# Performance work log

Hardware: AMD Instinct MI355X
Metric: run time of the kernel (lower is better)

## Reference

```python
import jax, jax.numpy as jnp
import numpy as np

B, N, HID = 4, 2048, 1024
QKV, NH = 1024, 16
HD = QKV // NH


def setup_inputs() -> dict:
    key = jax.random.key(0)
    ks = jax.random.split(key, 5)
    s = 1.0 / np.sqrt(HID)
    x = jax.random.normal(ks[0], (B, N, HID), dtype=jnp.float32)
    Wq = jax.random.normal(ks[1], (HID, QKV), dtype=jnp.float32) * s
    Wk = jax.random.normal(ks[2], (HID, QKV), dtype=jnp.float32) * s
    Wv = jax.random.normal(ks[3], (HID, QKV), dtype=jnp.float32) * s
    Wo = jax.random.normal(ks[4], (QKV, HID), dtype=jnp.float32) * (1.0 / np.sqrt(QKV))
    return {"x": x, "Wq": Wq, "Wk": Wk, "Wv": Wv, "Wo": Wo}


def reference(x, Wq, Wk, Wv, Wo):
    # Projections: [B, N, QKV]
    q = x @ Wq
    k = x @ Wk
    v = x @ Wv
    # Split heads -> [B, NH, N, HD]
    def split(t):
        return t.reshape(B, N, NH, HD).transpose(0, 2, 1, 3)
    q, k, v = split(q), split(k), split(v)
    # NOTE: original scales by 1/sqrt(qkv_dim) (full dim), not head_dim
    q = q * (1.0 / jnp.sqrt(jnp.float32(QKV)))
    scores = jnp.einsum("bhqd,bhkd->bhqk", q, k)  # [B, NH, N, N]
    attn = jax.nn.softmax(scores, axis=-1)
    out = jnp.einsum("bhqk,bhkd->bhqd", attn, v)  # [B, NH, N, HD]
    out = out.transpose(0, 2, 1, 3).reshape(B, N, QKV)
    return out @ Wo
```

## Files before the change

### kernel.cpp

```cpp
#include <hip/hip_runtime.h>

typedef unsigned short u16;
typedef unsigned int u32;
typedef __attribute__((ext_vector_type(8))) short bf16x8;
typedef __attribute__((ext_vector_type(4))) float f32x4;
typedef __attribute__((ext_vector_type(16))) float f32x16;

#define L2E 1.44269504088896340736f

__device__ __forceinline__ u16 f2bf(float f) {
  unsigned u = __float_as_uint(f);
  u += 0x7FFF + ((u >> 16) & 1u);
  return (u16)(u >> 16);
}

__device__ __forceinline__ u32 cvtpk(float lo, float hi) {
  u32 r;
  asm("v_cvt_pk_bf16_f32 %0, %1, %2" : "=v"(r) : "v"(lo), "v"(hi));
  return r;
}

__device__ __forceinline__ void gload_lds16(const u16* g, u16* lds) {
  __builtin_amdgcn_global_load_lds(
      (const __attribute__((address_space(1))) void*)g,
      (__attribute__((address_space(3))) void*)lds, 16, 0, 0);
}

__global__ __launch_bounds__(256) void k_cvt(const float* __restrict__ in,
                                             u16* __restrict__ out) {
  const int i = (blockIdx.x * 256 + threadIdx.x) * 4;
  float4 a = *(const float4*)(in + i);
  ushort4 o;
  o.x = f2bf(a.x); o.y = f2bf(a.y); o.z = f2bf(a.z); o.w = f2bf(a.w);
  *(ushort4*)(out + i) = o;
}

__global__ __launch_bounds__(256) void k_tw(
    const float* __restrict__ w0, const float* __restrict__ w1,
    const float* __restrict__ w2, const float* __restrict__ w3,
    u16* __restrict__ o0, u16* __restrict__ o1,
    u16* __restrict__ o2, u16* __restrict__ o3) {
  __shared__ float t[64][65];
  const float* W = blockIdx.z == 0 ? w0 : blockIdx.z == 1 ? w1 : blockIdx.z == 2 ? w2 : w3;
  u16* O = blockIdx.z == 0 ? o0 : blockIdx.z == 1 ? o1 : blockIdx.z == 2 ? o2 : o3;
  const int nb = blockIdx.x * 64, kb = blockIdx.y * 64;
  const int lx = threadIdx.x & 63, ly = threadIdx.x >> 6;
  for (int r = ly; r < 64; r += 4)
    t[r][lx] = W[(size_t)(kb + r) * 1024 + nb + lx];
  __syncthreads();
  for (int r = ly; r < 64; r += 4)
    O[(size_t)(nb + r) * 1024 + kb + lx] = f2bf(t[lx][r]);
}

__device__ __forceinline__ void gemm_core(const u16* __restrict__ Ag,
                                          const u16* __restrict__ Bg,
                                          f32x4 acc[4][4]) {
  __shared__ u16 As[4096], Bs[4096];
  const int tid = threadIdx.x;
  const int lane = tid & 63, wv = tid >> 6;
  const size_t row0 = (size_t)blockIdx.y * 128;
  const size_t col0 = (size_t)blockIdx.x * 128;
  const int rA0 = wv * 32 + (lane >> 2);
  const int rA1 = rA0 + 16;
  const int kk = (lane & 3) * 8;
  const int wr = (wv >> 1) * 64, wc = (wv & 1) * 64;
  const int fr = lane & 15, fk = (lane >> 4) * 8;
#pragma unroll
  for (int m = 0; m < 4; m++)
#pragma unroll
    for (int n = 0; n < 4; n++)
      acc[m][n] = {0.f, 0.f, 0.f, 0.f};

  for (int kt = 0; kt < 32; kt++) {
    const int k0 = kt * 32;
    gload_lds16(Ag + (row0 + rA0) * 1024 + k0 + kk, &As[(wv * 2 + 0) * 512]);
    gload_lds16(Ag + (row0 + rA1) * 1024 + k0 + kk, &As[(wv * 2 + 1) * 512]);
    gload_lds16(Bg + (col0 + rA0) * 1024 + k0 + kk, &Bs[(wv * 2 + 0) * 512]);
    gload_lds16(Bg + (col0 + rA1) * 1024 + k0 + kk, &Bs[(wv * 2 + 1) * 512]);
    __syncthreads();
    bf16x8 af[4], bfr[4];
#pragma unroll
    for (int m = 0; m < 4; m++)
      af[m] = *(const bf16x8*)&As[(wr + m * 16 + fr) * 32 + fk];
#pragma unroll
    for (int n = 0; n < 4; n++)
      bfr[n] = *(const bf16x8*)&Bs[(wc + n * 16 + fr) * 32 + fk];
#pragma unroll
    for (int m = 0; m < 4; m++)
#pragma unroll
      for (int n = 0; n < 4; n++)
        acc[m][n] = __builtin_amdgcn_mfma_f32_16x16x32_bf16(af[m], bfr[n], acc[m][n], 0, 0, 0);
    __syncthreads();
  }
}

__global__ __launch_bounds__(256) void k_proj(
    const u16* __restrict__ xb, const u16* __restrict__ wqT,
    const u16* __restrict__ wkT, const u16* __restrict__ wvT,
    u16* __restrict__ q, u16* __restrict__ k, u16* __restrict__ v) {
  f32x4 acc[4][4];
  const int z = blockIdx.z;
  const u16* Bg = z == 0 ? wqT : z == 1 ? wkT : wvT;
  gemm_core(xb, Bg, acc);
  const int lane = threadIdx.x & 63, wv = threadIdx.x >> 6;
  const int wr = (wv >> 1) * 64, wc = (wv & 1) * 64;
  const int rb = blockIdx.y * 128 + wr + ((lane >> 4) * 4);
  const int cb = blockIdx.x * 128 + wc + (lane & 15);
#pragma unroll
  for (int m = 0; m < 4; m++) {
#pragma unroll
    for (int n = 0; n < 4; n++) {
      const int C = cb + n * 16;
      const int h = C >> 6, d = C & 63;
      if (z == 2) {
        const int R = rb + m * 16;
        const int b = R >> 11, nn = R & 2047;
        ushort4 o;
        o.x = f2bf(acc[m][n][0]); o.y = f2bf(acc[m][n][1]);
        o.z = f2bf(acc[m][n][2]); o.w = f2bf(acc[m][n][3]);
        *(ushort4*)&v[(size_t)((b * 16 + h) * 64 + d) * 2048 + nn] = o;
      } else {
        u16* dst = (z == 0) ? q : k;
        const float s = (z == 0) ? (0.03125f * L2E) : 1.0f;
#pragma unroll
        for (int i = 0; i < 4; i++) {
          const int R = rb + m * 16 + i;
          const int b = R >> 11, nn = R & 2047;
          dst[(size_t)((b * 16 + h) * 2048 + nn) * 64 + d] = f2bf(acc[m][n][i] * s);
        }
      }
    }
  }
}

__global__ __launch_bounds__(256) void k_out(const u16* __restrict__ att,
                                             const u16* __restrict__ woT,
                                             float* __restrict__ out) {
  f32x4 acc[4][4];
  gemm_core(att, woT, acc);
  const int lane = threadIdx.x & 63, wv = threadIdx.x >> 6;
  const int wr = (wv >> 1) * 64, wc = (wv & 1) * 64;
  const int rb = blockIdx.y * 128 + wr + ((lane >> 4) * 4);
  const int cb = blockIdx.x * 128 + wc + (lane & 15);
#pragma unroll
  for (int m = 0; m < 4; m++)
#pragma unroll
    for (int n = 0; n < 4; n++)
#pragma unroll
      for (int i = 0; i < 4; i++)
        out[(size_t)(rb + m * 16 + i) * 1024 + cb + n * 16] = acc[m][n][i];
}

__global__ __launch_bounds__(256, 2) void k_attn(const u16* __restrict__ q,
                                                 const u16* __restrict__ k,
                                                 const u16* __restrict__ v,
                                                 u16* __restrict__ att) {
  __shared__ u16 SM[16384];
  const int lane = threadIdx.x & 63, wv = threadIdx.x >> 6;
  const int lo5 = lane & 31, hi = lane >> 5;
  const int r7 = lo5 & 7;
  const int bh = blockIdx.y;
  const int b = bh >> 4, h = bh & 15;
  const int q0w = blockIdx.x * 128 + wv * 32;
  const size_t base = (size_t)bh * 2048 * 64;

  const int l0 = wv * 64 + lane, l1 = 256 + l0;
  const int sr0 = l0 >> 3, sc0 = ((l0 & 7) ^ (sr0 & 7)) * 8;
  const int sr1 = l1 >> 3, sc1 = ((l1 & 7) ^ (sr1 & 7)) * 8;

  bf16x8 qb[4];
  {
    const u16* qp = q + base + (size_t)(q0w + lo5) * 64 + hi * 8;
#pragma unroll
    for (int db = 0; db < 4; db++) qb[db] = *(const bf16x8*)(qp + db * 16);
  }

  f32x16 o0, o1;
#pragma unroll
  for (int i = 0; i < 16; i++) { o0[i] = 0.f; o1[i] = 0.f; }
  float m_run = -3.0e38f, l_run = 0.f;

  {
    u16* Kd = SM;
    u16* Vd = SM + 4096;
    gload_lds16(k + base + (size_t)sr0 * 64 + sc0, Kd + wv * 512);
    gload_lds16(k + base + (size_t)sr1 * 64 + sc1, Kd + 2048 + wv * 512);
    gload_lds16(v + base + (size_t)sr0 * 2048 + sc0, Vd + wv * 512);
    gload_lds16(v + base + (size_t)sr1 * 2048 + sc1, Vd + 2048 + wv * 512);
  }
  __syncthreads();

  int cur = 0;
  for (int kt = 0; kt < 32; kt++) {
    const int kb = kt * 64;
    {
      const int nkb = (kt + 1 < 32 ? kt + 1 : 0) * 64;
      u16* Kd = SM + (cur ^ 1) * 8192;
      u16* Vd = Kd + 4096;
      gload_lds16(k + base + (size_t)(nkb + sr0) * 64 + sc0, Kd + wv * 512);
      gload_lds16(k + base + (size_t)(nkb + sr1) * 64 + sc1, Kd + 2048 + wv * 512);
      gload_lds16(v + base + (size_t)sr0 * 2048 + nkb + sc0, Vd + wv * 512);
      gload_lds16(v + base + (size_t)sr1 * 2048 + nkb + sc1, Vd + 2048 + wv * 512);
    }

    const u16* Kc = SM + cur * 8192;
    const u16* Vc = Kc + 4096;

    f32x16 s0, s1;
#pragma unroll
    for (int i = 0; i < 16; i++) { s0[i] = 0.f; s1[i] = 0.f; }
    __builtin_amdgcn_s_setprio(1);
#pragma unroll
    for (int db = 0; db < 4; db++) {
      const int swz = ((db * 2 + hi) ^ r7) << 3;
      const bf16x8 k0 = *(const bf16x8*)&Kc[lo5 * 64 + swz];
      const bf16x8 k1 = *(const bf16x8*)&Kc[(32 + lo5) * 64 + swz];
      s0 = __builtin_amdgcn_mfma_f32_32x32x16_bf16(k0, qb[db], s0, 0, 0, 0);
      s1 = __builtin_amdgcn_mfma_f32_32x32x16_bf16(k1, qb[db], s1, 0, 0, 0);
    }
    __builtin_amdgcn_s_setprio(0);

    float t[16];
#pragma unroll
    for (int i = 0; i < 16; i++) t[i] = fmaxf(s0[i], s1[i]);
#pragma unroll
    for (int off = 8; off; off >>= 1)
#pragma unroll
      for (int i = 0; i < off; i++) t[i] = fmaxf(t[i], t[i + off]);
    const float tmax = fmaxf(t[0], __shfl_xor(t[0], 32, 64));

    const bool skip = __all(tmax - m_run <= 8.0f);
    float sc = 1.0f;
    if (!skip) {
      const float mnew = fmaxf(m_run, tmax);
      sc = exp2f(m_run - mnew);
      m_run = mnew;
    }

    float p0[16], p1[16];
#pragma unroll
    for (int i = 0; i < 16; i++) {
      p0[i] = exp2f(s0[i] - m_run);
      p1[i] = exp2f(s1[i] - m_run);
    }
    float u[16];
#pragma unroll
    for (int i = 0; i < 16; i++) u[i] = p0[i] + p1[i];
#pragma unroll
    for (int off = 8; off; off >>= 1)
#pragma unroll
      for (int i = 0; i < off; i++) u[i] += u[i + off];
    const float rs = u[0] + __shfl_xor(u[0], 32, 64);
    l_run = l_run * sc + rs;
    if (!skip) {
#pragma unroll
      for (int i = 0; i < 16; i++) { o0[i] *= sc; o1[i] *= sc; }
    }

    bf16x8 pa[4];
#pragma unroll
    for (int kh = 0; kh < 2; kh++) {
      const float* pp = kh ? p1 : p0;
#pragma unroll
      for (int kl = 0; kl < 2; kl++) {
        const int r0 = kl * 8;
        const u32 a0 = cvtpk(pp[r0 + 0], pp[r0 + 1]);
        const u32 a1 = cvtpk(pp[r0 + 2], pp[r0 + 3]);
        const u32 b0 = cvtpk(pp[r0 + 4], pp[r0 + 5]);
        const u32 b1 = cvtpk(pp[r0 + 6], pp[r0 + 7]);
        const u32 a0x = (u32)__shfl_xor((int)a0, 32, 64);
        const u32 a1x = (u32)__shfl_xor((int)a1, 32, 64);
        const u32 b0x = (u32)__shfl_xor((int)b0, 32, 64);
        const u32 b1x = (u32)__shfl_xor((int)b1, 32, 64);
        union { u32 w[4]; bf16x8 v; } U;
        U.w[0] = hi ? b0x : a0;
        U.w[1] = hi ? b1x : a1;
        U.w[2] = hi ? b0 : a0x;
        U.w[3] = hi ? b1 : a1x;
        pa[kh * 2 + kl] = U.v;
      }
    }

    __builtin_amdgcn_s_setprio(1);
#pragma unroll
    for (int ks = 0; ks < 4; ks++) {
      const int swz = ((ks * 2 + hi) ^ r7) << 3;
      const bf16x8 v0 = *(const bf16x8*)&Vc[lo5 * 64 + swz];
      const bf16x8 v1 = *(const bf16x8*)&Vc[(32 + lo5) * 64 + swz];
      o0 = __builtin_amdgcn_mfma_f32_32x32x16_bf16(v0, pa[ks], o0, 0, 0, 0);
      o1 = __builtin_amdgcn_mfma_f32_32x32x16_bf16(v1, pa[ks], o1, 0, 0, 0);
    }
    __builtin_amdgcn_s_setprio(0);

    __syncthreads();
    cur ^= 1;
  }

  const float linv = 1.0f / l_run;
  u16* W = SM + wv * 2176;
#pragma unroll
  for (int r = 0; r < 16; r++) {
    const int dd = (r & 3) + 8 * (r >> 2) + 4 * hi;
    W[lo5 * 68 + dd] = f2bf(o0[r] * linv);
    W[lo5 * 68 + 32 + dd] = f2bf(o1[r] * linv);
  }
  const int q_loc = lane >> 1, dh = (lane & 1) * 32;
  u16* dst = att + (size_t)(b * 2048 + q0w + q_loc) * 1024 + h * 64 + dh;
#pragma unroll
  for (int c = 0; c < 4; c++) {
    bf16x8 val = *(const bf16x8*)&W[q_loc * 68 + dh + c * 8];
    *(bf16x8*)(dst + c * 8) = val;
  }
}

extern "C" void kernel_launch(void* const* d_in, const int* in_sizes, int n_in,
                              void* d_out, int out_size, void* d_ws, size_t ws_size,
                              hipStream_t stream) {
  const float* x  = (const float*)d_in[0];
  const float* Wq = (const float*)d_in[1];
  const float* Wk = (const float*)d_in[2];
  const float* Wv = (const float*)d_in[3];
  const float* Wo = (const float*)d_in[4];
  float* out = (float*)d_out;

  char* ws = (char*)d_ws;
  u16* xb  = (u16*)ws; ws += (size_t)8192 * 1024 * 2;
  u16* wqT = (u16*)ws; ws += (size_t)1024 * 1024 * 2;
  u16* wkT = (u16*)ws; ws += (size_t)1024 * 1024 * 2;
  u16* wvT = (u16*)ws; ws += (size_t)1024 * 1024 * 2;
  u16* woT = (u16*)ws; ws += (size_t)1024 * 1024 * 2;
  u16* qb  = (u16*)ws; ws += (size_t)8192 * 1024 * 2;
  u16* kb  = (u16*)ws; ws += (size_t)8192 * 1024 * 2;
  u16* vb  = (u16*)ws; ws += (size_t)8192 * 1024 * 2;
  u16* att = (u16*)ws; ws += (size_t)8192 * 1024 * 2;

  k_cvt<<<dim3(8192), dim3(256), 0, stream>>>(x, xb);
  k_tw<<<dim3(16, 16, 4), dim3(256), 0, stream>>>(Wq, Wk, Wv, Wo, wqT, wkT, wvT, woT);
  k_proj<<<dim3(8, 64, 3), dim3(256), 0, stream>>>(xb, wqT, wkT, wvT, qb, kb, vb);
  k_attn<<<dim3(16, 64), dim3(256), 0, stream>>>(qb, kb, vb, att);
  k_out<<<dim3(8, 64), dim3(256), 0, stream>>>(att, woT, out);
}
```

Baseline: 351.9 us.

## Pre-tile K/V in LDS-ready layout, defer row-sum reduction, use native exp2

The QKV projection now writes K and V into a pre-tiled, fragment-ordered layout for each 64-key block. The attention kernel can then fetch each tile with contiguous global-to-LDS loads and read MFMA operands with simple strided offsets, with no XOR swizzle. The softmax denominator is kept as 16 per-lane partial sums and reduced only once after the loop, which removes a reduction tree and shuffle from every iteration. exp2f is replaced with the hardware exp2 builtin. The main risk is LDS bank conflicts from the unswizzled strided reads.

```diff
diff --git a/kernel.cpp b/kernel.cpp
--- a/kernel.cpp
+++ b/kernel.cpp
@@ -115,18 +115,30 @@
       if (z == 2) {
         const int R = rb + m * 16;
         const int b = R >> 11, nn = R & 2047;
+        const int bh = b * 16 + h;
         ushort4 o;
         o.x = f2bf(acc[m][n][0]); o.y = f2bf(acc[m][n][1]);
         o.z = f2bf(acc[m][n][2]); o.w = f2bf(acc[m][n][3]);
-        *(ushort4*)&v[(size_t)((b * 16 + h) * 64 + d) * 2048 + nn] = o;
-      } else {
-        u16* dst = (z == 0) ? q : k;
-        const float s = (z == 0) ? (0.03125f * L2E) : 1.0f;
+        const size_t off = (size_t)bh * 131072 + (size_t)(nn >> 6) * 4096 +
+                           ((nn & 63) >> 3) * 512 + d * 8 + (nn & 7);
+        *(ushort4*)&v[off] = o;
+      } else if (z == 1) {
 #pragma unroll
         for (int i = 0; i < 4; i++) {
           const int R = rb + m * 16 + i;
           const int b = R >> 11, nn = R & 2047;
-          dst[(size_t)((b * 16 + h) * 2048 + nn) * 64 + d] = f2bf(acc[m][n][i] * s);
+          const int bh = b * 16 + h;
+          const size_t off = (size_t)bh * 131072 + (size_t)(nn >> 6) * 4096 +
+                             (d >> 3) * 512 + (nn & 63) * 8 + (d & 7);
+          k[off] = f2bf(acc[m][n][i]);
+        }
+      } else {
+        const float s = 0.03125f * L2E;
+#pragma unroll
+        for (int i = 0; i < 4; i++) {
+          const int R = rb + m * 16 + i;
+          const int b = R >> 11, nn = R & 2047;
+          q[(size_t)((b * 16 + h) * 2048 + nn) * 64 + d] = f2bf(acc[m][n][i] * s);
         }
       }
     }
@@ -151,26 +163,24 @@
         out[(size_t)(rb + m * 16 + i) * 1024 + cb + n * 16] = acc[m][n][i];
 }
 
-__global__ __launch_bounds__(256, 2) void k_attn(const u16* __restrict__ q,
-                                                 const u16* __restrict__ k,
-                                                 const u16* __restrict__ v,
+__global__ __launch_bounds__(256, 2) void k_attn(const u16* __restrict__ qg,
+                                                 const u16* __restrict__ kg,
+                                                 const u16* __restrict__ vg,
                                                  u16* __restrict__ att) {
   __shared__ u16 SM[16384];
-  const int lane = threadIdx.x & 63, wv = threadIdx.x >> 6;
+  const int tid = threadIdx.x;
+  const int lane = tid & 63, wv = tid >> 6;
   const int lo5 = lane & 31, hi = lane >> 5;
-  const int r7 = lo5 & 7;
   const int bh = blockIdx.y;
   const int b = bh >> 4, h = bh & 15;
   const int q0w = blockIdx.x * 128 + wv * 32;
-  const size_t base = (size_t)bh * 2048 * 64;
-
-  const int l0 = wv * 64 + lane, l1 = 256 + l0;
-  const int sr0 = l0 >> 3, sc0 = ((l0 & 7) ^ (sr0 & 7)) * 8;
-  const int sr1 = l1 >> 3, sc1 = ((l1 & 7) ^ (sr1 & 7)) * 8;
+  const size_t qbase = (size_t)bh * 2048 * 64;
+  const u16* kt0 = kg + (size_t)bh * 131072;
+  const u16* vt0 = vg + (size_t)bh * 131072;
 
   bf16x8 qb[4];
   {
-    const u16* qp = q + base + (size_t)(q0w + lo5) * 64 + hi * 8;
+    const u16* qp = qg + qbase + (size_t)(q0w + lo5) * 64 + hi * 8;
 #pragma unroll
     for (int db = 0; db < 4; db++) qb[db] = *(const bf16x8*)(qp + db * 16);
   }
@@ -178,32 +188,31 @@
   f32x16 o0, o1;
 #pragma unroll
   for (int i = 0; i < 16; i++) { o0[i] = 0.f; o1[i] = 0.f; }
-  float m_run = -3.0e38f, l_run = 0.f;
-
-  {
-    u16* Kd = SM;
-    u16* Vd = SM + 4096;
-    gload_lds16(k + base + (size_t)sr0 * 64 + sc0, Kd + wv * 512);
-    gload_lds16(k + base + (size_t)sr1 * 64 + sc1, Kd + 2048 + wv * 512);
-    gload_lds16(v + base + (size_t)sr0 * 2048 + sc0, Vd + wv * 512);
-    gload_lds16(v + base + (size_t)sr1 * 2048 + sc1, Vd + 2048 + wv * 512);
-  }
+  float m_run = -3.0e38f;
+  float l16[16];
+#pragma unroll
+  for (int i = 0; i < 16; i++) l16[i] = 0.f;
+
+  gload_lds16(kt0 + (size_t)tid * 8, SM + wv * 512);
+  gload_lds16(kt0 + (size_t)(256 + tid) * 8, SM + 2048 + wv * 512);
+  gload_lds16(vt0 + (size_t)tid * 8, SM + 4096 + wv * 512);
+  gload_lds16(vt0 + (size_t)(256 + tid) * 8, SM + 6144 + wv * 512);
   __syncthreads();
 
   int cur = 0;
-  for (int kt = 0; kt < 32; kt++) {
-    const int kb = kt * 64;
+  for (int t = 0; t < 32; t++) {
     {
-      const int nkb = (kt + 1 < 32 ? kt + 1 : 0) * 64;
+      const int nt = (t + 1) & 31;
+      const u16* ks = kt0 + (size_t)nt * 4096;
+      const u16* vs = vt0 + (size_t)nt * 4096;
       u16* Kd = SM + (cur ^ 1) * 8192;
-      u16* Vd = Kd + 4096;
-      gload_lds16(k + base + (size_t)(nkb + sr0) * 64 + sc0, Kd + wv * 512);
-      gload_lds16(k + base + (size_t)(nkb + sr1) * 64 + sc1, Kd + 2048 + wv * 512);
-      gload_lds16(v + base + (size_t)sr0 * 2048 + nkb + sc0, Vd + wv * 512);
-      gload_lds16(v + base + (size_t)sr1 * 2048 + nkb + sc1, Vd + 2048 + wv * 512);
-    }
-
-    const u16* Kc = SM + cur * 8192;
+      gload_lds16(ks + (size_t)tid * 8, Kd + wv * 512);
+      gload_lds16(ks + (size_t)(256 + tid) * 8, Kd + 2048 + wv * 512);
+      gload_lds16(vs + (size_t)tid * 8, Kd + 4096 + wv * 512);
+      gload_lds16(vs + (size_t)(256 + tid) * 8, Kd + 6144 + wv * 512);
+    }
+
+    const u16* Kc = SM + cur * 8192 + hi * 512 + lo5 * 8;
     const u16* Vc = Kc + 4096;
 
     f32x16 s0, s1;
@@ -212,49 +221,39 @@
     __builtin_amdgcn_s_setprio(1);
 #pragma unroll
     for (int db = 0; db < 4; db++) {
-      const int swz = ((db * 2 + hi) ^ r7) << 3;
-      const bf16x8 k0 = *(const bf16x8*)&Kc[lo5 * 64 + swz];
-      const bf16x8 k1 = *(const bf16x8*)&Kc[(32 + lo5) * 64 + swz];
+      const bf16x8 k0 = *(const bf16x8*)&Kc[db * 1024];
+      const bf16x8 k1 = *(const bf16x8*)&Kc[db * 1024 + 256];
       s0 = __builtin_amdgcn_mfma_f32_32x32x16_bf16(k0, qb[db], s0, 0, 0, 0);
       s1 = __builtin_amdgcn_mfma_f32_32x32x16_bf16(k1, qb[db], s1, 0, 0, 0);
     }
     __builtin_amdgcn_s_setprio(0);
 
-    float t[16];
-#pragma unroll
-    for (int i = 0; i < 16; i++) t[i] = fmaxf(s0[i], s1[i]);
+    float tmx[16];
+#pragma unroll
+    for (int i = 0; i < 16; i++) tmx[i] = fmaxf(s0[i], s1[i]);
 #pragma unroll
     for (int off = 8; off; off >>= 1)
 #pragma unroll
-      for (int i = 0; i < off; i++) t[i] = fmaxf(t[i], t[i + off]);
-    const float tmax = fmaxf(t[0], __shfl_xor(t[0], 32, 64));
+      for (int i = 0; i < off; i++) tmx[i] = fmaxf(tmx[i], tmx[i + off]);
+    const float tmax = fmaxf(tmx[0], __shfl_xor(tmx[0], 32, 64));
 
     const bool skip = __all(tmax - m_run <= 8.0f);
-    float sc = 1.0f;
     if (!skip) {
       const float mnew = fmaxf(m_run, tmax);
-      sc = exp2f(m_run - mnew);
+      const float sc = __builtin_amdgcn_exp2f(m_run - mnew);
       m_run = mnew;
+#pragma unroll
+      for (int i = 0; i < 16; i++) {
+        l16[i] *= sc; o0[i] *= sc; o1[i] *= sc;
+      }
     }
 
     float p0[16], p1[16];
 #pragma unroll
     for (int i = 0; i < 16; i++) {
-      p0[i] = exp2f(s0[i] - m_run);
-      p1[i] = exp2f(s1[i] - m_run);
-    }
-    float u[16];
-#pragma unroll
-    for (int i = 0; i < 16; i++) u[i] = p0[i] + p1[i];
-#pragma unroll
-    for (int off = 8; off; off >>= 1)
-#pragma unroll
-      for (int i = 0; i < off; i++) u[i] += u[i + off];
-    const float rs = u[0] + __shfl_xor(u[0], 32, 64);
-    l_run = l_run * sc + rs;
-    if (!skip) {
-#pragma unroll
-      for (int i = 0; i < 16; i++) { o0[i] *= sc; o1[i] *= sc; }
+      p0[i] = __builtin_amdgcn_exp2f(s0[i] - m_run);
+      p1[i] = __builtin_amdgcn_exp2f(s1[i] - m_run);
+      l16[i] += p0[i] + p1[i];
     }
 
     bf16x8 pa[4];
@@ -284,9 +283,8 @@
     __builtin_amdgcn_s_setprio(1);
 #pragma unroll
     for (int ks = 0; ks < 4; ks++) {
-      const int swz = ((ks * 2 + hi) ^ r7) << 3;
-      const bf16x8 v0 = *(const bf16x8*)&Vc[lo5 * 64 + swz];
-      const bf16x8 v1 = *(const bf16x8*)&Vc[(32 + lo5) * 64 + swz];
+      const bf16x8 v0 = *(const bf16x8*)&Vc[ks * 1024];
+      const bf16x8 v1 = *(const bf16x8*)&Vc[ks * 1024 + 256];
       o0 = __builtin_amdgcn_mfma_f32_32x32x16_bf16(v0, pa[ks], o0, 0, 0, 0);
       o1 = __builtin_amdgcn_mfma_f32_32x32x16_bf16(v1, pa[ks], o1, 0, 0, 0);
     }
@@ -296,7 +294,16 @@
     cur ^= 1;
   }
 
-  const float linv = 1.0f / l_run;
+  float ls[8];
+#pragma unroll
+  for (int i = 0; i < 8; i++) ls[i] = l16[i] + l16[i + 8];
+#pragma unroll
+  for (int off = 4; off; off >>= 1)
+#pragma unroll
+    for (int i = 0; i < off; i++) ls[i] += ls[i + off];
+  const float lsum = ls[0] + __shfl_xor(ls[0], 32, 64);
+  const float linv = 1.0f / lsum;
+
   u16* W = SM + wv * 2176;
 #pragma unroll
   for (int r = 0; r < 16; r++) {
```

Measured after the change: 316.5 us. 10.0% less time.
